# Optimization experiments

Measured on AMD Instinct MI355X. Metric: run time of the kernel, lower is better.

Reference implementation:

```python
import jax, jax.numpy as jnp
import numpy as np

B, T, H = 256, 1024, 128

def _lstm_cell(x, h, c, W_ih, W_hh, b_ih, b_hh):
    # PyTorch LSTMCell gate order: i, f, g, o
    gates = x @ W_ih.T + b_ih + h @ W_hh.T + b_hh  # [B, 4H]
    i, f, g, o = jnp.split(gates, 4, axis=-1)
    c_new = jax.nn.sigmoid(f) * c + jax.nn.sigmoid(i) * jnp.tanh(g)
    h_new = jax.nn.sigmoid(o) * jnp.tanh(c_new)
    return h_new, c_new

def setup_inputs() -> dict:
    key = jax.random.key(0)
    ks = jax.random.split(key, 12)
    s = 1.0 / np.sqrt(H)
    u = lambda k, shape: jax.random.uniform(k, shape, jnp.float32, -s, s)
    return {
        "x": jax.random.normal(ks[0], (B, T, 1), jnp.float32),
        "W_ih1": u(ks[1], (4 * H, 1)),
        "W_hh1": u(ks[2], (4 * H, H)),
        "b_ih1": u(ks[3], (4 * H,)),
        "b_hh1": u(ks[4], (4 * H,)),
        "W_ih2": u(ks[5], (4 * H, H)),
        "W_hh2": u(ks[6], (4 * H, H)),
        "b_ih2": u(ks[7], (4 * H,)),
        "b_hh2": u(ks[8], (4 * H,)),
        "W_out": u(ks[9], (1, H)),
        "b_out": u(ks[10], (1,)),
    }

def reference(x, W_ih1, W_hh1, b_ih1, b_hh1, W_ih2, W_hh2, b_ih2, b_hh2, W_out, b_out):
    n = x.shape[0]
    z = jnp.zeros((n, H), jnp.float32)

    def step(carry, x_t):  # x_t: [B, 1]
        h1, c1, h2, c2 = carry
        h1, c1 = _lstm_cell(x_t, h1, c1, W_ih1, W_hh1, b_ih1, b_hh1)
        h2, c2 = _lstm_cell(h1, h2, c2, W_ih2, W_hh2, b_ih2, b_hh2)
        out = h2 @ W_out.T + b_out  # [B, 1]
        return (h1, c1, h2, c2), out

    xs = jnp.transpose(x, (1, 0, 2))  # [T, B, 1]
    _, outs = jax.lax.scan(step, (z, z, z, z), xs)  # outs: [T, B, 1]
    return jnp.transpose(outs[..., 0], (1, 0))  # [B, T]
```

## Files before the change

### kernel.cpp

```cpp
#include <hip/hip_runtime.h>
#include <hip/hip_fp16.h>
#include <stdint.h>

#define T_STEPS 1024
#define HDIM    128
#define NT      512


typedef _Float16 v2h __attribute__((ext_vector_type(2)));
union HU { uint32_t u; v2h v; };

__device__ __forceinline__ float dot2h(uint32_t a, uint32_t b, float c) {
    HU ua, ub; ua.u = a; ub.u = b;
    return __builtin_amdgcn_fdot2(ua.v, ub.v, c, false);
}
__device__ __forceinline__ uint32_t packh2f(float2 e) {
    return (uint32_t)__half_as_ushort(__float2half_rn(e.x)) |
           ((uint32_t)__half_as_ushort(__float2half_rn(e.y)) << 16);
}
__device__ __forceinline__ uint16_t f2h(float f) {
    return __half_as_ushort(__float2half_rn(f));
}
__device__ __forceinline__ float actf(float a, float m) {
    return 1.0f - m * __builtin_amdgcn_rcpf(__expf(m * a) + 1.0f);
}

__device__ __forceinline__ float red2(float v) {
    int iv = __float_as_int(v);
    v += __int_as_float(__builtin_amdgcn_update_dpp(0, iv, 0xB1, 0xF, 0xF, true));
    iv = __float_as_int(v);
    v += __int_as_float(__builtin_amdgcn_update_dpp(0, iv, 0x4E, 0xF, 0xF, true));
    return v;
}

#define SB() __builtin_amdgcn_sched_barrier(0)
#define PIN4(W) asm volatile("" : "+v"(W.x), "+v"(W.y), "+v"(W.z), "+v"(W.w))

#define SETW16(Wa, Wb, Wc, Wd, P) do { const float2* _r = (const float2*)(P); \
    Wa = make_uint4(packh2f(_r[0]),  packh2f(_r[1]),                       \
                    packh2f(_r[2]),  packh2f(_r[3]));                      \
    Wb = make_uint4(packh2f(_r[4]),  packh2f(_r[5]),                       \
                    packh2f(_r[6]),  packh2f(_r[7]));                      \
    Wc = make_uint4(packh2f(_r[8]),  packh2f(_r[9]),                       \
                    packh2f(_r[10]), packh2f(_r[11]));                     \
    Wd = make_uint4(packh2f(_r[12]), packh2f(_r[13]),                      \
                    packh2f(_r[14]), packh2f(_r[15])); } while (0)

#define DOT8(Wa, Wb, H0, H1, acc) do {                                     \
    acc = dot2h(Wa.x, H0.x, acc); acc = dot2h(Wa.y, H0.y, acc);            \
    acc = dot2h(Wa.z, H0.z, acc); acc = dot2h(Wa.w, H0.w, acc);            \
    acc = dot2h(Wb.x, H1.x, acc); acc = dot2h(Wb.y, H1.y, acc);            \
    acc = dot2h(Wb.z, H1.z, acc); acc = dot2h(Wb.w, H1.w, acc); } while (0)

#define DOT16(W0, W1, W2, W3, H0, H1, H2, H3, acc) do {                    \
    DOT8(W0, W1, H0, H1, acc); DOT8(W2, W3, H2, H3, acc); } while (0)

__global__ __launch_bounds__(NT)
__attribute__((amdgpu_waves_per_eu(2, 2)))
void lstm_persistent(
    const float* __restrict__ x,
    const float* __restrict__ W_ih1, const float* __restrict__ W_hh1,
    const float* __restrict__ b_ih1, const float* __restrict__ b_hh1,
    const float* __restrict__ W_ih2, const float* __restrict__ W_hh2,
    const float* __restrict__ b_ih2, const float* __restrict__ b_hh2,
    const float* __restrict__ W_out, const float* __restrict__ b_out,
    float* __restrict__ out)
{
    const int b   = blockIdx.x;
    const int tid = threadIdx.x;
    const int w   = tid >> 6;
    const int l   = tid & 63;
    const int s   = l & 3;
    const int e   = (w << 4) | (l >> 2);
    const int co  = s << 5;

    __shared__ __align__(16) uint32_t h1p[2][HDIM / 2];
    __shared__ __align__(16) uint32_t h2p[2][HDIM / 2];
    __shared__ float pbuf[8];

    uint4 m1_00,m1_01,m1_02,m1_03, m1_10,m1_11,m1_12,m1_13;
    uint4 m1_20,m1_21,m1_22,m1_23, m1_30,m1_31,m1_32,m1_33;
    uint4 m2_00,m2_01,m2_02,m2_03, m2_10,m2_11,m2_12,m2_13;
    uint4 m2_20,m2_21,m2_22,m2_23, m2_30,m2_31,m2_32,m2_33;
    uint4 m3_00,m3_01,m3_02,m3_03, m3_10,m3_11,m3_12,m3_13;
    uint4 m3_20,m3_21,m3_22,m3_23, m3_30,m3_31,m3_32,m3_33;
    {
        const float* p = W_hh1 + e * HDIM + co;
        SETW16(m1_00,m1_01,m1_02,m1_03, p);
        SETW16(m1_10,m1_11,m1_12,m1_13, p + 128 * HDIM);
        SETW16(m1_20,m1_21,m1_22,m1_23, p + 256 * HDIM);
        SETW16(m1_30,m1_31,m1_32,m1_33, p + 384 * HDIM);
        p = W_ih2 + e * HDIM + co;
        SETW16(m2_00,m2_01,m2_02,m2_03, p);
        SETW16(m2_10,m2_11,m2_12,m2_13, p + 128 * HDIM);
        SETW16(m2_20,m2_21,m2_22,m2_23, p + 256 * HDIM);
        SETW16(m2_30,m2_31,m2_32,m2_33, p + 384 * HDIM);
        p = W_hh2 + e * HDIM + co;
        SETW16(m3_00,m3_01,m3_02,m3_03, p);
        SETW16(m3_10,m3_11,m3_12,m3_13, p + 128 * HDIM);
        SETW16(m3_20,m3_21,m3_22,m3_23, p + 256 * HDIM);
        SETW16(m3_30,m3_31,m3_32,m3_33, p + 384 * HDIM);
    }
    PIN4(m1_00); PIN4(m1_01); PIN4(m1_02); PIN4(m1_03);
    PIN4(m1_10); PIN4(m1_11); PIN4(m1_12); PIN4(m1_13);
    PIN4(m1_20); PIN4(m1_21); PIN4(m1_22); PIN4(m1_23);
    PIN4(m1_30); PIN4(m1_31); PIN4(m1_32); PIN4(m1_33);
    PIN4(m2_00); PIN4(m2_01); PIN4(m2_02); PIN4(m2_03);
    PIN4(m2_10); PIN4(m2_11); PIN4(m2_12); PIN4(m2_13);
    PIN4(m2_20); PIN4(m2_21); PIN4(m2_22); PIN4(m2_23);
    PIN4(m2_30); PIN4(m2_31); PIN4(m2_32); PIN4(m2_33);
    PIN4(m3_00); PIN4(m3_01); PIN4(m3_02); PIN4(m3_03);
    PIN4(m3_10); PIN4(m3_11); PIN4(m3_12); PIN4(m3_13);
    PIN4(m3_20); PIN4(m3_21); PIN4(m3_22); PIN4(m3_23);
    PIN4(m3_30); PIN4(m3_31); PIN4(m3_32); PIN4(m3_33);

    const float b1i = b_ih1[e]       + b_hh1[e];
    const float b1f = b_ih1[e + 128] + b_hh1[e + 128];
    const float b1g = b_ih1[e + 256] + b_hh1[e + 256];
    const float b1o = b_ih1[e + 384] + b_hh1[e + 384];
    const float wxi = W_ih1[e],      wxf = W_ih1[e + 128];
    const float wxg = W_ih1[e + 256], wxo = W_ih1[e + 384];
    const float b2i = b_ih2[e]       + b_hh2[e];
    const float b2f = b_ih2[e + 128] + b_hh2[e + 128];
    const float b2g = b_ih2[e + 256] + b_hh2[e + 256];
    const float b2o = b_ih2[e + 384] + b_hh2[e + 384];
    const float wo  = (s == 0) ? W_out[e] : 0.0f;
    const float bo  = b_out[0];

    float c1 = 0.f, c2 = 0.f;

    if (tid < HDIM / 2) {
        h1p[0][tid] = 0u; h1p[1][tid] = 0u;
        h2p[0][tid] = 0u; h2p[1][tid] = 0u;
    }
    __syncthreads();

    const float* xb = x + b * T_STEPS;
    float*       ob = out + b * T_STEPS;
    float x_cur = xb[0];

    for (int t = 0; t < T_STEPS; t++) {
        const int rb = t & 1, wb2 = rb ^ 1;
        float x_nxt = xb[(t + 1 < T_STEPS) ? (t + 1) : t];

        float a0 = 0.f, a1 = 0.f, a2 = 0.f, a3 = 0.f;
        {
            const uint4* H = (const uint4*)h1p[rb];
            uint4 H0 = H[4*s], H1 = H[4*s+1], H2 = H[4*s+2], H3 = H[4*s+3];
            DOT16(m1_00,m1_01,m1_02,m1_03, H0,H1,H2,H3, a0);
            DOT16(m1_10,m1_11,m1_12,m1_13, H0,H1,H2,H3, a1);
            DOT16(m1_20,m1_21,m1_22,m1_23, H0,H1,H2,H3, a2);
            DOT16(m1_30,m1_31,m1_32,m1_33, H0,H1,H2,H3, a3);
        }
        a0 = red2(a0); a1 = red2(a1); a2 = red2(a2); a3 = red2(a3);
        float gi = actf(a0 + fmaf(x_cur, wxi, b1i), 1.0f);
        float gf = actf(a1 + fmaf(x_cur, wxf, b1f), 1.0f);
        float gg = actf(a2 + fmaf(x_cur, wxg, b1g), 2.0f);
        float go = actf(a3 + fmaf(x_cur, wxo, b1o), 1.0f);
        c1 = fmaf(gf, c1, gi * gg);
        float h1 = go * actf(c1, 2.0f);
        if (s == 0) ((uint16_t*)h1p[wb2])[e] = f2h(h1);
        __syncthreads();

        float q0 = 0.f, q1 = 0.f, q2 = 0.f, q3 = 0.f;
        {
            const uint4* Hn = (const uint4*)h1p[wb2];
            uint4 G0 = Hn[4*s], G1 = Hn[4*s+1], G2 = Hn[4*s+2], G3 = Hn[4*s+3];
            DOT16(m2_00,m2_01,m2_02,m2_03, G0,G1,G2,G3, q0);
            DOT16(m2_10,m2_11,m2_12,m2_13, G0,G1,G2,G3, q1);
            DOT16(m2_20,m2_21,m2_22,m2_23, G0,G1,G2,G3, q2);
            DOT16(m2_30,m2_31,m2_32,m2_33, G0,G1,G2,G3, q3);
        }
        SB();
        {
            const uint4* Ho = (const uint4*)h2p[rb];
            uint4 G0 = Ho[4*s], G1 = Ho[4*s+1], G2 = Ho[4*s+2], G3 = Ho[4*s+3];
            DOT16(m3_00,m3_01,m3_02,m3_03, G0,G1,G2,G3, q0);
            DOT16(m3_10,m3_11,m3_12,m3_13, G0,G1,G2,G3, q1);
            DOT16(m3_20,m3_21,m3_22,m3_23, G0,G1,G2,G3, q2);
            DOT16(m3_30,m3_31,m3_32,m3_33, G0,G1,G2,G3, q3);
        }
        q0 = red2(q0); q1 = red2(q1); q2 = red2(q2); q3 = red2(q3);
        float hi = actf(q0 + b2i, 1.0f);
        float hf = actf(q1 + b2f, 1.0f);
        float hg = actf(q2 + b2g, 2.0f);
        float ho = actf(q3 + b2o, 1.0f);
        c2 = fmaf(hf, c2, hi * hg);
        float h2v = ho * actf(c2, 2.0f);
        if (s == 0) ((uint16_t*)h2p[wb2])[e] = f2h(h2v);

        float part = wo * h2v;
        part += __shfl_xor(part, 4,  64);
        part += __shfl_xor(part, 8,  64);
        part += __shfl_xor(part, 16, 64);
        part += __shfl_xor(part, 32, 64);
        if (l == 0) pbuf[w] = part;
        __syncthreads();

        if (tid < 8) {
            float ssum = pbuf[tid];
            ssum += __shfl_xor(ssum, 1, 64);
            ssum += __shfl_xor(ssum, 2, 64);
            ssum += __shfl_xor(ssum, 4, 64);
            if (tid == 0) ob[t] = ssum + bo;
        }
        x_cur = x_nxt;
    }
}

extern "C" void kernel_launch(void* const* d_in, const int* in_sizes, int n_in,
                              void* d_out, int out_size, void* d_ws, size_t ws_size,
                              hipStream_t stream) {
    const float* x     = (const float*)d_in[0];
    const float* W_ih1 = (const float*)d_in[1];
    const float* W_hh1 = (const float*)d_in[2];
    const float* b_ih1 = (const float*)d_in[3];
    const float* b_hh1 = (const float*)d_in[4];
    const float* W_ih2 = (const float*)d_in[5];
    const float* W_hh2 = (const float*)d_in[6];
    const float* b_ih2 = (const float*)d_in[7];
    const float* b_hh2 = (const float*)d_in[8];
    const float* W_out = (const float*)d_in[9];
    const float* b_out = (const float*)d_in[10];
    float* out = (float*)d_out;

    const int B = in_sizes[0] / T_STEPS;
    hipLaunchKernelGGL(lstm_persistent, dim3(B), dim3(NT), 0, stream,
                       x, W_ih1, W_hh1, b_ih1, b_hh1,
                       W_ih2, W_hh2, b_ih2, b_hh2, W_out, b_out, out);
}
```

Before: 1.699 ms.

## Skew layer-2 LSTM one step behind layer-1 to use one barrier per step

Restructures the time loop so layer 1 at step k and layer 2 at step k-1 are computed together from the same shared h1 buffer. Each iteration then needs one __syncthreads instead of two, and the two layers' dot products interleave for more ILP. The final output reduction is deferred one iteration, with an epilogue for the last step. Biases and input weights move from registers into shared-memory float4 tables to cut register pressure, at the cost of extra LDS reads per step. Weight loading now places a sched barrier after each row.

```diff
diff --git a/kernel.cpp b/kernel.cpp
--- a/kernel.cpp
+++ b/kernel.cpp
@@ -24,7 +24,6 @@
 __device__ __forceinline__ float actf(float a, float m) {
     return 1.0f - m * __builtin_amdgcn_rcpf(__expf(m * a) + 1.0f);
 }
-
 __device__ __forceinline__ float red2(float v) {
     int iv = __float_as_int(v);
     v += __int_as_float(__builtin_amdgcn_update_dpp(0, iv, 0xB1, 0xF, 0xF, true));
@@ -46,14 +45,15 @@
     Wd = make_uint4(packh2f(_r[12]), packh2f(_r[13]),                      \
                     packh2f(_r[14]), packh2f(_r[15])); } while (0)
 
+#define ROW(Wa, Wb, Wc, Wd, P) do {                                        \
+    SETW16(Wa, Wb, Wc, Wd, P);                                             \
+    PIN4(Wa); PIN4(Wb); PIN4(Wc); PIN4(Wd); SB(); } while (0)
+
 #define DOT8(Wa, Wb, H0, H1, acc) do {                                     \
     acc = dot2h(Wa.x, H0.x, acc); acc = dot2h(Wa.y, H0.y, acc);            \
     acc = dot2h(Wa.z, H0.z, acc); acc = dot2h(Wa.w, H0.w, acc);            \
     acc = dot2h(Wb.x, H1.x, acc); acc = dot2h(Wb.y, H1.y, acc);            \
     acc = dot2h(Wb.z, H1.z, acc); acc = dot2h(Wb.w, H1.w, acc); } while (0)
-
-#define DOT16(W0, W1, W2, W3, H0, H1, H2, H3, acc) do {                    \
-    DOT8(W0, W1, H0, H1, acc); DOT8(W2, W3, H2, H3, acc); } while (0)
 
 __global__ __launch_bounds__(NT)
 __attribute__((amdgpu_waves_per_eu(2, 2)))
@@ -76,7 +76,10 @@
 
     __shared__ __align__(16) uint32_t h1p[2][HDIM / 2];
     __shared__ __align__(16) uint32_t h2p[2][HDIM / 2];
-    __shared__ float pbuf[8];
+    __shared__ __align__(16) float4 bct1[HDIM];
+    __shared__ __align__(16) float4 bctw[HDIM];
+    __shared__ __align__(16) float4 bct2[HDIM];
+    __shared__ float pbuf[2][8];
 
     uint4 m1_00,m1_01,m1_02,m1_03, m1_10,m1_11,m1_12,m1_13;
     uint4 m1_20,m1_21,m1_22,m1_23, m1_30,m1_31,m1_32,m1_33;
@@ -86,46 +89,38 @@
     uint4 m3_20,m3_21,m3_22,m3_23, m3_30,m3_31,m3_32,m3_33;
     {
         const float* p = W_hh1 + e * HDIM + co;
-        SETW16(m1_00,m1_01,m1_02,m1_03, p);
-        SETW16(m1_10,m1_11,m1_12,m1_13, p + 128 * HDIM);
-        SETW16(m1_20,m1_21,m1_22,m1_23, p + 256 * HDIM);
-        SETW16(m1_30,m1_31,m1_32,m1_33, p + 384 * HDIM);
+        ROW(m1_00,m1_01,m1_02,m1_03, p);
+        ROW(m1_10,m1_11,m1_12,m1_13, p + 128 * HDIM);
+        ROW(m1_20,m1_21,m1_22,m1_23, p + 256 * HDIM);
+        ROW(m1_30,m1_31,m1_32,m1_33, p + 384 * HDIM);
         p = W_ih2 + e * HDIM + co;
-        SETW16(m2_00,m2_01,m2_02,m2_03, p);
-        SETW16(m2_10,m2_11,m2_12,m2_13, p + 128 * HDIM);
-        SETW16(m2_20,m2_21,m2_22,m2_23, p + 256 * HDIM);
-        SETW16(m2_30,m2_31,m2_32,m2_33, p + 384 * HDIM);
+        ROW(m2_00,m2_01,m2_02,m2_03, p);
+        ROW(m2_10,m2_11,m2_12,m2_13, p + 128 * HDIM);
+        ROW(m2_20,m2_21,m2_22,m2_23, p + 256 * HDIM);
+        ROW(m2_30,m2_31,m2_32,m2_33, p + 384 * HDIM);
         p = W_hh2 + e * HDIM + co;
-        SETW16(m3_00,m3_01,m3_02,m3_03, p);
-        SETW16(m3_10,m3_11,m3_12,m3_13, p + 128 * HDIM);
-        SETW16(m3_20,m3_21,m3_22,m3_23, p + 256 * HDIM);
-        SETW16(m3_30,m3_31,m3_32,m3_33, p + 384 * HDIM);
-    }
-    PIN4(m1_00); PIN4(m1_01); PIN4(m1_02); PIN4(m1_03);
-    PIN4(m1_10); PIN4(m1_11); PIN4(m1_12); PIN4(m1_13);
-    PIN4(m1_20); PIN4(m1_21); PIN4(m1_22); PIN4(m1_23);
-    PIN4(m1_30); PIN4(m1_31); PIN4(m1_32); PIN4(m1_33);
-    PIN4(m2_00); PIN4(m2_01); PIN4(m2_02); PIN4(m2_03);
-    PIN4(m2_10); PIN4(m2_11); PIN4(m2_12); PIN4(m2_13);
-    PIN4(m2_20); PIN4(m2_21); PIN4(m2_22); PIN4(m2_23);
-    PIN4(m2_30); PIN4(m2_31); PIN4(m2_32); PIN4(m2_33);
-    PIN4(m3_00); PIN4(m3_01); PIN4(m3_02); PIN4(m3_03);
-    PIN4(m3_10); PIN4(m3_11); PIN4(m3_12); PIN4(m3_13);
-    PIN4(m3_20); PIN4(m3_21); PIN4(m3_22); PIN4(m3_23);
-    PIN4(m3_30); PIN4(m3_31); PIN4(m3_32); PIN4(m3_33);
-
-    const float b1i = b_ih1[e]       + b_hh1[e];
-    const float b1f = b_ih1[e + 128] + b_hh1[e + 128];
-    const float b1g = b_ih1[e + 256] + b_hh1[e + 256];
-    const float b1o = b_ih1[e + 384] + b_hh1[e + 384];
-    const float wxi = W_ih1[e],      wxf = W_ih1[e + 128];
-    const float wxg = W_ih1[e + 256], wxo = W_ih1[e + 384];
-    const float b2i = b_ih2[e]       + b_hh2[e];
-    const float b2f = b_ih2[e + 128] + b_hh2[e + 128];
-    const float b2g = b_ih2[e + 256] + b_hh2[e + 256];
-    const float b2o = b_ih2[e + 384] + b_hh2[e + 384];
-    const float wo  = (s == 0) ? W_out[e] : 0.0f;
-    const float bo  = b_out[0];
+        ROW(m3_00,m3_01,m3_02,m3_03, p);
+        ROW(m3_10,m3_11,m3_12,m3_13, p + 128 * HDIM);
+        ROW(m3_20,m3_21,m3_22,m3_23, p + 256 * HDIM);
+        ROW(m3_30,m3_31,m3_32,m3_33, p + 384 * HDIM);
+    }
+
+    if (tid < HDIM) {
+        bct1[tid] = make_float4(
+            b_ih1[tid]       + b_hh1[tid],
+            b_ih1[tid + 128] + b_hh1[tid + 128],
+            b_ih1[tid + 256] + b_hh1[tid + 256],
+            b_ih1[tid + 384] + b_hh1[tid + 384]);
+        bctw[tid] = make_float4(W_ih1[tid], W_ih1[tid + 128],
+                                W_ih1[tid + 256], W_ih1[tid + 384]);
+        bct2[tid] = make_float4(
+            b_ih2[tid]       + b_hh2[tid],
+            b_ih2[tid + 128] + b_hh2[tid + 128],
+            b_ih2[tid + 256] + b_hh2[tid + 256],
+            b_ih2[tid + 384] + b_hh2[tid + 384]);
+    }
+    const float wo = (s == 0) ? W_out[e] : 0.0f;
+    const float bo = b_out[0];
 
     float c1 = 0.f, c2 = 0.f;
 
@@ -139,72 +134,78 @@
     float*       ob = out + b * T_STEPS;
     float x_cur = xb[0];
 
-    for (int t = 0; t < T_STEPS; t++) {
-        const int rb = t & 1, wb2 = rb ^ 1;
-        float x_nxt = xb[(t + 1 < T_STEPS) ? (t + 1) : t];
-
-        float a0 = 0.f, a1 = 0.f, a2 = 0.f, a3 = 0.f;
-        {
-            const uint4* H = (const uint4*)h1p[rb];
-            uint4 H0 = H[4*s], H1 = H[4*s+1], H2 = H[4*s+2], H3 = H[4*s+3];
-            DOT16(m1_00,m1_01,m1_02,m1_03, H0,H1,H2,H3, a0);
-            DOT16(m1_10,m1_11,m1_12,m1_13, H0,H1,H2,H3, a1);
-            DOT16(m1_20,m1_21,m1_22,m1_23, H0,H1,H2,H3, a2);
-            DOT16(m1_30,m1_31,m1_32,m1_33, H0,H1,H2,H3, a3);
-        }
-        a0 = red2(a0); a1 = red2(a1); a2 = red2(a2); a3 = red2(a3);
-        float gi = actf(a0 + fmaf(x_cur, wxi, b1i), 1.0f);
-        float gf = actf(a1 + fmaf(x_cur, wxf, b1f), 1.0f);
-        float gg = actf(a2 + fmaf(x_cur, wxg, b1g), 2.0f);
-        float go = actf(a3 + fmaf(x_cur, wxo, b1o), 1.0f);
-        c1 = fmaf(gf, c1, gi * gg);
-        float h1 = go * actf(c1, 2.0f);
-        if (s == 0) ((uint16_t*)h1p[wb2])[e] = f2h(h1);
-        __syncthreads();
-
-        float q0 = 0.f, q1 = 0.f, q2 = 0.f, q3 = 0.f;
-        {
-            const uint4* Hn = (const uint4*)h1p[wb2];
-            uint4 G0 = Hn[4*s], G1 = Hn[4*s+1], G2 = Hn[4*s+2], G3 = Hn[4*s+3];
-            DOT16(m2_00,m2_01,m2_02,m2_03, G0,G1,G2,G3, q0);
-            DOT16(m2_10,m2_11,m2_12,m2_13, G0,G1,G2,G3, q1);
-            DOT16(m2_20,m2_21,m2_22,m2_23, G0,G1,G2,G3, q2);
-            DOT16(m2_30,m2_31,m2_32,m2_33, G0,G1,G2,G3, q3);
-        }
-        SB();
-        {
-            const uint4* Ho = (const uint4*)h2p[rb];
-            uint4 G0 = Ho[4*s], G1 = Ho[4*s+1], G2 = Ho[4*s+2], G3 = Ho[4*s+3];
-            DOT16(m3_00,m3_01,m3_02,m3_03, G0,G1,G2,G3, q0);
-            DOT16(m3_10,m3_11,m3_12,m3_13, G0,G1,G2,G3, q1);
-            DOT16(m3_20,m3_21,m3_22,m3_23, G0,G1,G2,G3, q2);
-            DOT16(m3_30,m3_31,m3_32,m3_33, G0,G1,G2,G3, q3);
-        }
-        q0 = red2(q0); q1 = red2(q1); q2 = red2(q2); q3 = red2(q3);
-        float hi = actf(q0 + b2i, 1.0f);
-        float hf = actf(q1 + b2f, 1.0f);
-        float hg = actf(q2 + b2g, 2.0f);
-        float ho = actf(q3 + b2o, 1.0f);
-        c2 = fmaf(hf, c2, hi * hg);
-        float h2v = ho * actf(c2, 2.0f);
-        if (s == 0) ((uint16_t*)h2p[wb2])[e] = f2h(h2v);
-
-        float part = wo * h2v;
-        part += __shfl_xor(part, 4,  64);
-        part += __shfl_xor(part, 8,  64);
-        part += __shfl_xor(part, 16, 64);
-        part += __shfl_xor(part, 32, 64);
-        if (l == 0) pbuf[w] = part;
-        __syncthreads();
-
-        if (tid < 8) {
-            float ssum = pbuf[tid];
+    for (int k = 0; k <= T_STEPS; ++k) {
+        const int rb = k & 1, wbuf = rb ^ 1;
+        float x_nxt = xb[(k + 1 < T_STEPS) ? (k + 1) : (T_STEPS - 1)];
+
+        if (k >= 2 && tid < 8) {
+            float ssum = pbuf[wbuf][tid];
             ssum += __shfl_xor(ssum, 1, 64);
             ssum += __shfl_xor(ssum, 2, 64);
             ssum += __shfl_xor(ssum, 4, 64);
-            if (tid == 0) ob[t] = ssum + bo;
+            if (tid == 0) ob[k - 2] = ssum + bo;
         }
+
+        const uint4* H1 = (const uint4*)h1p[rb];
+        const uint4* H2 = (const uint4*)h2p[rb];
+        uint4 Ha0 = H1[4*s+0], Ha1 = H1[4*s+1];
+        uint4 Hb0 = H1[4*s+2], Hb1 = H1[4*s+3];
+        uint4 Hc0 = H2[4*s+0], Hc1 = H2[4*s+1];
+        uint4 Hd0 = H2[4*s+2], Hd1 = H2[4*s+3];
+        float a0=0.f,a1=0.f,a2=0.f,a3=0.f, q0=0.f,q1=0.f,q2=0.f,q3=0.f;
+        DOT8(m1_00,m1_01, Ha0,Ha1, a0); DOT8(m1_10,m1_11, Ha0,Ha1, a1);
+        DOT8(m1_20,m1_21, Ha0,Ha1, a2); DOT8(m1_30,m1_31, Ha0,Ha1, a3);
+        DOT8(m2_00,m2_01, Ha0,Ha1, q0); DOT8(m2_10,m2_11, Ha0,Ha1, q1);
+        DOT8(m2_20,m2_21, Ha0,Ha1, q2); DOT8(m2_30,m2_31, Ha0,Ha1, q3);
+        DOT8(m1_02,m1_03, Hb0,Hb1, a0); DOT8(m1_12,m1_13, Hb0,Hb1, a1);
+        DOT8(m1_22,m1_23, Hb0,Hb1, a2); DOT8(m1_32,m1_33, Hb0,Hb1, a3);
+        DOT8(m2_02,m2_03, Hb0,Hb1, q0); DOT8(m2_12,m2_13, Hb0,Hb1, q1);
+        DOT8(m2_22,m2_23, Hb0,Hb1, q2); DOT8(m2_32,m2_33, Hb0,Hb1, q3);
+        DOT8(m3_00,m3_01, Hc0,Hc1, q0); DOT8(m3_10,m3_11, Hc0,Hc1, q1);
+        DOT8(m3_20,m3_21, Hc0,Hc1, q2); DOT8(m3_30,m3_31, Hc0,Hc1, q3);
+        DOT8(m3_02,m3_03, Hd0,Hd1, q0); DOT8(m3_12,m3_13, Hd0,Hd1, q1);
+        DOT8(m3_22,m3_23, Hd0,Hd1, q2); DOT8(m3_32,m3_33, Hd0,Hd1, q3);
+
+        int ei = e;
+        asm volatile("" : "+v"(ei));
+        float4 B1 = bct1[ei];
+        float4 Wx = bctw[ei];
+        a0 = red2(a0); a1 = red2(a1); a2 = red2(a2); a3 = red2(a3);
+        float gi = actf(a0 + fmaf(x_cur, Wx.x, B1.x), 1.0f);
+        float gf = actf(a1 + fmaf(x_cur, Wx.y, B1.y), 1.0f);
+        float gg = actf(a2 + fmaf(x_cur, Wx.z, B1.z), 2.0f);
+        float go = actf(a3 + fmaf(x_cur, Wx.w, B1.w), 1.0f);
+        c1 = fmaf(gf, c1, gi * gg);
+        float h1v = go * actf(c1, 2.0f);
+        if (s == 0) ((uint16_t*)h1p[wbuf])[e] = f2h(h1v);
+
+        if (k > 0) {
+            float4 B2 = bct2[ei];
+            q0 = red2(q0); q1 = red2(q1); q2 = red2(q2); q3 = red2(q3);
+            float hi = actf(q0 + B2.x, 1.0f);
+            float hf = actf(q1 + B2.y, 1.0f);
+            float hg = actf(q2 + B2.z, 2.0f);
+            float ho = actf(q3 + B2.w, 1.0f);
+            c2 = fmaf(hf, c2, hi * hg);
+            float h2v = ho * actf(c2, 2.0f);
+            if (s == 0) ((uint16_t*)h2p[wbuf])[e] = f2h(h2v);
+            float part = wo * h2v;
+            part += __shfl_xor(part, 4,  64);
+            part += __shfl_xor(part, 8,  64);
+            part += __shfl_xor(part, 16, 64);
+            part += __shfl_xor(part, 32, 64);
+            if (l == 0) pbuf[rb][w] = part;
+        }
+        __syncthreads();
         x_cur = x_nxt;
+    }
+
+    if (tid < 8) {
+        float ssum = pbuf[T_STEPS & 1][tid];
+        ssum += __shfl_xor(ssum, 1, 64);
+        ssum += __shfl_xor(ssum, 2, 64);
+        ssum += __shfl_xor(ssum, 4, 64);
+        if (tid == 0) ob[T_STEPS - 1] = ssum + bo;
     }
 }
 
```

After: 1.589 ms. -6.5%, faster.
